# Optimization experiments

Hardware: AMD Instinct MI355X
Metric: run time of the kernel (lower is better)

## Reference

```python
import jax, jax.numpy as jnp
import numpy as np
from jax import lax

B, W, M = 4, 20, 512
RNN_HID = 64
N_HIDDEN = RNN_HID          # bi = False
HALF = N_HIDDEN // 2
K = 10
LONG_K = W // 2             # conv_long kernel
LONG_OUT = W - 2 * (LONG_K - 1)   # = 2
N_SPATIAL = 10


def setup_inputs() -> dict:
    key = jax.random.key(0)
    ks = jax.random.split(key, 24)
    g = lambda i, shape, s=0.05: jax.random.normal(ks[i], shape, jnp.float32) * s
    return {
        "x": jax.random.normal(ks[0], (B, W, M), jnp.float32),
        # vanilla RNN (tanh), 1 layer, input_size=1
        "W_ih": g(1, (RNN_HID, 1), 0.2), "W_hh": g(2, (RNN_HID, RNN_HID), 0.1),
        "b_ih": g(3, (RNN_HID,)), "b_hh": g(4, (RNN_HID,)),
        # attention adjacency params
        "W1": g(5, (HALF, N_HIDDEN), 0.1), "b1": g(6, (HALF,)),
        "W2": g(7, (HALF, N_HIDDEN), 0.1),
        "V": g(8, (HALF,), 0.1), "bv": g(9, (1,)),
        "Wb": g(10, (M, M), 0.05), "wb": g(11, (1,)),
        # conv / conv_long
        "conv_w": g(12, (K, 1, W), 0.1), "conv_b": g(13, (K,)),
        "convl_w": g(14, (K, 1, LONG_K), 0.1), "convl_b": g(15, (K,)),
        # graph conv layers: adj @ (x @ W) + b
        "gc1_w": g(16, ((1 + LONG_OUT) * K, N_HIDDEN), 0.1), "gc1_b": g(17, (N_HIDDEN,)),
        "gc2_w": g(18, (N_HIDDEN, N_SPATIAL), 0.1), "gc2_b": g(19, (N_SPATIAL,)),
        # output head
        "out_w": g(20, (1, N_HIDDEN + N_SPATIAL), 0.1), "out_b": g(21, (1,)),
        # fixed geographic adjacency (data.adj)
        "adj": jax.random.uniform(ks[22], (M, M), dtype=jnp.float32),
    }


def _conv1d(x, w, b, dilation=1):
    # x: (N, Cin, W), w: (Cout, Cin, K) -> (N, Cout, Wout), VALID padding
    y = lax.conv_general_dilated(x, w, (1,), 'VALID', rhs_dilation=(dilation,),
                                 dimension_numbers=('NCH', 'OIH', 'NCH'))
    return y + b[None, :, None]


def reference(x, W_ih, W_hh, b_ih, b_hh, W1, b1, W2, V, bv, Wb, wb,
              conv_w, conv_b, convl_w, convl_b, gc1_w, gc1_b, gc2_w, gc2_b,
              out_w, out_b, adj):
    b, w, m = x.shape
    # ---- RNN encode each node's scalar series: (b*m, w, 1) -> last hidden ----
    xr = jnp.transpose(x, (0, 2, 1)).reshape(b * m, w)          # (bm, w)
    inp = xr[..., None] @ W_ih.T + b_ih                         # (bm, w, H)

    def step(h, u):
        return jnp.tanh(u + h @ W_hh.T + b_hh), None

    h0 = jnp.zeros((b * m, RNN_HID), x.dtype)
    h_last, _ = lax.scan(step, h0, jnp.swapaxes(inp, 0, 1))     # (bm, H)
    last_hid = h_last.reshape(b, m, N_HIDDEN)
    out_temporal = last_hid

    # ---- pairwise bilinear attention adjacency (broadcast instead of repeat) ----
    p = last_hid @ W1.T                                         # (b, m, H/2)
    q = last_hid @ W2.T                                         # (b, m, H/2)
    e = jax.nn.elu(p[:, :, None, :] + q[:, None, :, :] + b1)    # (b, m, m, H/2)
    a_mx = e @ V + bv[0]                                        # (b, m, m)
    # F.normalize(p=2, dim=1)
    nrm = jnp.maximum(jnp.sqrt(jnp.sum(a_mx * a_mx, axis=1, keepdims=True)), 1e-12)
    a_mx = a_mx / nrm
    c = jax.nn.sigmoid(a_mx @ Wb + wb[0])                       # (b, m, m)
    A = adj[None] * c + a_mx * (1.0 - c)

    # ---- per-node convs, batched over all b*m series (no Python loop) ----
    h_tmp = xr[:, None, :]                                      # (bm, 1, w)
    r = _conv1d(h_tmp, conv_w, conv_b)                          # (bm, k, 1)
    r_long = _conv1d(h_tmp, convl_w, convl_b, dilation=2)       # (bm, k, long_out)
    r_l = jnp.concatenate([r, r_long], axis=-1).reshape(b, m, -1)  # (b, m, (1+lo)*k)
    r_l = jax.nn.relu(r_l)

    # ---- graph convolutions: adj @ (x @ W) + b ----
    xg = jax.nn.relu(A @ (r_l @ gc1_w) + gc1_b)                 # (b, m, H)
    out_spatial = jax.nn.relu(A @ (xg @ gc2_w) + gc2_b)         # (b, m, 10)

    out = jnp.concatenate([out_spatial, out_temporal], axis=-1)
    return (out @ out_w.T + out_b)[..., 0]                      # (b, m)
```

## Files before the change

kernel.cpp:

```cpp
#include <hip/hip_runtime.h>
#include <hip/hip_bf16.h>
#include <cstdint>
#include <cstddef>

#define OFF_P     0
#define OFF_QB    65536
#define OFF_TDOT  131072
#define OFF_COLSQ 133120
#define OFF_XGP   135168
#define OFF_AMXB  266240
#define OFF_ABF   790528
#define OFF_G1T   1314816
#define OFF_WBT   1380352

typedef __attribute__((ext_vector_type(8))) short short8;
typedef __attribute__((ext_vector_type(8))) unsigned short ushort8;
typedef __attribute__((ext_vector_type(4))) float f32x4;

__device__ inline unsigned short f2bf(float f) {
    unsigned u = __builtin_bit_cast(unsigned, f);
    unsigned r = u + 0x7FFFu + ((u >> 16) & 1u);
    return (unsigned short)(r >> 16);
}
__device__ inline unsigned short f2bf_fast(float f) {
    unsigned u = __builtin_bit_cast(unsigned, f);
    return (unsigned short)((u + 0x8000u) >> 16);
}
__device__ inline float bf2f(unsigned short s) {
    unsigned u = ((unsigned)s) << 16;
    return __builtin_bit_cast(float, u);
}
__device__ inline float tanh_fast(float x) {
    return 1.f - 2.f/(__expf(2.f*x) + 1.f);
}

__global__ __launch_bounds__(256) void k1_rnn(
    const float* __restrict__ x, const float* __restrict__ W_ih,
    const float* __restrict__ W_hh, const float* __restrict__ b_ih,
    const float* __restrict__ b_hh, const float* __restrict__ W1,
    const float* __restrict__ b1, const float* __restrict__ W2,
    const float* __restrict__ conv_w, const float* __restrict__ conv_b,
    const float* __restrict__ convl_w, const float* __restrict__ convl_b,
    const float* __restrict__ gc1_w, const float* __restrict__ out_w,
    const float* __restrict__ out_b, const float* __restrict__ Wb,
    float* __restrict__ p_out, float* __restrict__ qb_out,
    unsigned short* __restrict__ G1T, float* __restrict__ tdot,
    float* __restrict__ colsq, unsigned short* __restrict__ WbT)
{
    __shared__ float h_sh[4][64];
    __shared__ float xt_sh[4][20];
    __shared__ float rl_sh[4][30];
    __shared__ float tile[64][68];
    int tid = threadIdx.x;

    if (blockIdx.x >= 512) {
        int tt = blockIdx.x - 512;
        int k0 = (tt >> 3) * 64, j0 = (tt & 7) * 64;
        #pragma unroll
        for (int q = 0; q < 4; ++q) {
            int kr = (tid>>4) + 16*q;
            int jc = (tid&15)*4;
            *(float4*)&tile[kr][jc] = *(const float4*)(Wb + (size_t)(k0+kr)*512 + j0 + jc);
        }
        __syncthreads();
        int jl = tid>>2, kc = (tid&3)*16;
        int j = j0 + jl;
        ushort8 v0, v1;
        #pragma unroll
        for (int kk = 0; kk < 8; ++kk) v0[kk] = f2bf(tile[kc+kk][jl]);
        #pragma unroll
        for (int kk = 0; kk < 8; ++kk) v1[kk] = f2bf(tile[kc+8+kk][jl]);
        unsigned short* dst = WbT + (size_t)j*512 + k0 + kc;
        *(ushort8*)dst = v0;
        *(ushort8*)(dst+8) = v1;
        return;
    }

    int w = tid >> 6, lane = tid & 63;
    int s = blockIdx.x * 4 + w;
    int b = s >> 9, m = s & 511;

    if (blockIdx.x < 8) colsq[blockIdx.x * 256 + tid] = 0.f;

    if (lane < 20) xt_sh[w][lane] = x[(b*20 + lane)*512 + m];

    float wrow[64];
    const float* wr = W_hh + lane*64;
    #pragma unroll
    for (int k4 = 0; k4 < 16; ++k4) {
        float4 v = reinterpret_cast<const float4*>(wr)[k4];
        wrow[4*k4+0]=v.x; wrow[4*k4+1]=v.y; wrow[4*k4+2]=v.z; wrow[4*k4+3]=v.w;
    }
    float wih = W_ih[lane], bih = b_ih[lane], bhh = b_hh[lane];
    h_sh[w][lane] = 0.f;
    float h = 0.f;

    if (lane < 10) {
        float acc = conv_b[lane];
        #pragma unroll
        for (int t = 0; t < 20; ++t) acc += conv_w[lane*20+t]*xt_sh[w][t];
        rl_sh[w][3*lane] = fmaxf(acc, 0.f);
    } else if (lane < 30) {
        int idx = lane-10, j = idx>>1, oo = idx&1;
        float acc = convl_b[j];
        #pragma unroll
        for (int t = 0; t < 10; ++t) acc += convl_w[j*10+t]*xt_sh[w][oo+2*t];
        rl_sh[w][3*j+1+oo] = fmaxf(acc, 0.f);
    }

    for (int t = 0; t < 20; ++t) {
        float a0=0.f, a1=0.f, a2=0.f, a3=0.f;
        #pragma unroll
        for (int k = 0; k < 64; k += 4) {
            a0 += wrow[k+0]*h_sh[w][k+0];
            a1 += wrow[k+1]*h_sh[w][k+1];
            a2 += wrow[k+2]*h_sh[w][k+2];
            a3 += wrow[k+3]*h_sh[w][k+3];
        }
        float acc = xt_sh[w][t]*wih + bih + bhh + ((a0+a1)+(a2+a3));
        h = tanh_fast(acc);
        h_sh[w][lane] = h;
    }

    float td = h * out_w[10 + lane];
    #pragma unroll
    for (int off = 32; off; off >>= 1) td += __shfl_down(td, off);
    if (lane == 0) tdot[s] = td + out_b[0];

    if (lane < 32) {
        const float* w1r = W1 + lane*64;
        float acc = 0.f;
        #pragma unroll
        for (int k = 0; k < 64; ++k) acc += w1r[k]*h_sh[w][k];
        p_out[s*32 + lane] = acc;
    } else {
        int i = lane - 32;
        const float* w2r = W2 + i*64;
        float acc = 0.f;
        #pragma unroll
        for (int k = 0; k < 64; ++k) acc += w2r[k]*h_sh[w][k];
        qb_out[s*32 + i] = acc + b1[i];
    }

    float g = 0.f;
    #pragma unroll
    for (int t = 0; t < 30; ++t) g += rl_sh[w][t]*gc1_w[t*64 + lane];
    G1T[((size_t)(b*64 + lane))*512 + m] = f2bf(g);
}

__global__ __launch_bounds__(256) void k2_amx(
    const float* __restrict__ p, const float* __restrict__ qb,
    const float* __restrict__ V, const float* __restrict__ bv,
    unsigned short* __restrict__ amxB, float* __restrict__ colsq,
    float* __restrict__ xg_pre)
{
    __shared__ float p_sh[32*36], q_sh[32*36], v_sh[32], sq_sh[32*17];
    int t = threadIdx.x;
    int b = blockIdx.z, i0 = blockIdx.y*32, j0 = blockIdx.x*32;

    int fb = (blockIdx.z<<8) | (blockIdx.y<<4) | blockIdx.x;
    if (fb < 128) {
        float4 zz = {0.f,0.f,0.f,0.f};
        *(float4*)&xg_pre[(size_t)fb*1024 + t*4] = zz;
    }

    {
        int r = t >> 3, c4 = (t & 7)*4;
        *(float4*)&p_sh[r*36 + c4] = *(const float4*)(p  + (size_t)(b*512 + i0 + r)*32 + c4);
        *(float4*)&q_sh[r*36 + c4] = *(const float4*)(qb + (size_t)(b*512 + j0 + r)*32 + c4);
    }
    if (t < 32) v_sh[t] = V[t];
    __syncthreads();

    int ti = t >> 4, tj = t & 15;
    float bv0 = bv[0];
    float a00 = bv0, a01 = bv0, a10 = bv0, a11 = bv0;
    #pragma unroll
    for (int h = 0; h < 32; ++h) {
        float p0 = p_sh[ti*36 + h], p1 = p_sh[(ti+16)*36 + h];
        float q0 = q_sh[tj*36 + h], q1 = q_sh[(tj+16)*36 + h];
        float vh = v_sh[h];
        float x00 = p0+q0, x01 = p0+q1, x10 = p1+q0, x11 = p1+q1;
        float e00 = x00 > 0.f ? x00 : __expf(x00)-1.f;
        float e01 = x01 > 0.f ? x01 : __expf(x01)-1.f;
        float e10 = x10 > 0.f ? x10 : __expf(x10)-1.f;
        float e11 = x11 > 0.f ? x11 : __expf(x11)-1.f;
        a00 += vh*e00; a01 += vh*e01; a10 += vh*e10; a11 += vh*e11;
    }
    size_t base0 = ((size_t)(b*512 + i0 + ti))*512 + j0;
    size_t base1 = ((size_t)(b*512 + i0 + ti + 16))*512 + j0;
    amxB[base0 + tj]      = f2bf(a00);
    amxB[base0 + tj + 16] = f2bf(a01);
    amxB[base1 + tj]      = f2bf(a10);
    amxB[base1 + tj + 16] = f2bf(a11);

    sq_sh[tj*17 + ti]      = a00*a00 + a10*a10;
    sq_sh[(tj+16)*17 + ti] = a01*a01 + a11*a11;
    __syncthreads();
    if (t < 32) {
        float ssum = 0.f;
        #pragma unroll
        for (int r = 0; r < 16; ++r) ssum += sq_sh[t*17 + r];
        atomicAdd(&colsq[b*512 + j0 + t], ssum);
    }
}

__global__ __launch_bounds__(256) void k3_mfma(
    const unsigned short* __restrict__ amxB, const unsigned short* __restrict__ WbT,
    const unsigned short* __restrict__ G1T, const float* __restrict__ colsq,
    const float* __restrict__ wb, const float* __restrict__ adj,
    unsigned short* __restrict__ Abf, float* __restrict__ xg_pre)
{
    __shared__ unsigned short amx_save[4][32*40];
    __shared__ unsigned short Atr[4][32*40];
    int tid = threadIdx.x;
    int wv = tid >> 6, lane = tid & 63;
    int b = blockIdx.z;
    int i0 = blockIdx.y*32;
    int j0 = blockIdx.x*128 + wv*32;

    f32x4 acc[2][2] = {};

    int sl = (lane>>4)*8;
    int fr = lane & 15;
    const unsigned short* abase = amxB + ((size_t)(b*512 + i0 + fr))*512 + sl;
    const unsigned short* bbase = WbT  + ((size_t)(j0 + fr))*512 + sl;
    const float* csq = colsq + b*512 + sl;

    #pragma unroll 2
    for (int k0 = 0; k0 < 512; k0 += 32) {
        float4 c0 = *(const float4*)(csq + k0);
        float4 c1 = *(const float4*)(csq + k0 + 4);
        float iv[8] = {
            rsqrtf(fmaxf(c0.x,1e-24f)), rsqrtf(fmaxf(c0.y,1e-24f)),
            rsqrtf(fmaxf(c0.z,1e-24f)), rsqrtf(fmaxf(c0.w,1e-24f)),
            rsqrtf(fmaxf(c1.x,1e-24f)), rsqrtf(fmaxf(c1.y,1e-24f)),
            rsqrtf(fmaxf(c1.z,1e-24f)), rsqrtf(fmaxf(c1.w,1e-24f)) };

        short8 a0r = *(const short8*)(abase + k0);
        short8 a1r = *(const short8*)(abase + 16*512 + k0);
        short8 b0  = *(const short8*)(bbase + k0);
        short8 b1  = *(const short8*)(bbase + 16*512 + k0);

        if (k0 == j0) {
            *(short8*)&amx_save[wv][fr*40 + sl]      = a0r;
            *(short8*)&amx_save[wv][(fr+16)*40 + sl] = a1r;
        }

        short8 a0, a1;
        #pragma unroll
        for (int e = 0; e < 8; ++e) {
            a0[e] = (short)f2bf_fast(bf2f((unsigned short)a0r[e]) * iv[e]);
            a1[e] = (short)f2bf_fast(bf2f((unsigned short)a1r[e]) * iv[e]);
        }

        acc[0][0] = __builtin_amdgcn_mfma_f32_16x16x32_bf16(a0, b0, acc[0][0],0,0,0);
        acc[0][1] = __builtin_amdgcn_mfma_f32_16x16x32_bf16(a0, b1, acc[0][1],0,0,0);
        acc[1][0] = __builtin_amdgcn_mfma_f32_16x16x32_bf16(a1, b0, acc[1][0],0,0,0);
        acc[1][1] = __builtin_amdgcn_mfma_f32_16x16x32_bf16(a1, b1, acc[1][1],0,0,0);
    }

    float wbs = wb[0];
    #pragma unroll
    for (int fj = 0; fj < 2; ++fj) {
        int jl = fj*16 + fr;
        int j = j0 + jl;
        float inv = rsqrtf(fmaxf(colsq[b*512 + j], 1e-24f));
        #pragma unroll
        for (int fi = 0; fi < 2; ++fi)
        #pragma unroll
        for (int r = 0; r < 4; ++r) {
            int il = fi*16 + (lane>>4)*4 + r;
            float S = acc[fi][fj][r] + wbs;
            float c = 1.f/(1.f + __expf(-S));
            float aN = bf2f(amx_save[wv][il*40 + jl]) * inv;
            unsigned short u = f2bf(adj[(size_t)(i0+il)*512 + j]*c + aN*(1.f - c));
            Abf[((size_t)(b*512) + i0 + il)*512 + j] = u;
            Atr[wv][il*40 + jl] = u;
        }
    }

    short8 aT0 = *(const short8*)&Atr[wv][fr*40 + sl];
    short8 aT1 = *(const short8*)&Atr[wv][(fr+16)*40 + sl];
    f32x4 acc2[2][4] = {};
    #pragma unroll
    for (int cb = 0; cb < 4; ++cb) {
        short8 gfrag = *(const short8*)(G1T + ((size_t)(b*64 + cb*16 + fr))*512 + j0 + sl);
        acc2[0][cb] = __builtin_amdgcn_mfma_f32_16x16x32_bf16(aT0, gfrag, acc2[0][cb],0,0,0);
        acc2[1][cb] = __builtin_amdgcn_mfma_f32_16x16x32_bf16(aT1, gfrag, acc2[1][cb],0,0,0);
    }
    #pragma unroll
    for (int fi = 0; fi < 2; ++fi)
    #pragma unroll
    for (int cb = 0; cb < 4; ++cb)
    #pragma unroll
    for (int rr = 0; rr < 4; ++rr) {
        int i = i0 + fi*16 + (lane>>4)*4 + rr;
        int c = cb*16 + fr;
        atomicAdd(&xg_pre[((size_t)(b*512) + i)*64 + c], acc2[fi][cb][rr]);
    }
}

__global__ __launch_bounds__(256) void k4_out(
    const unsigned short* __restrict__ Abf, const float* __restrict__ xg_pre,
    const float* __restrict__ gc1_b, const float* __restrict__ gc2_w,
    const float* __restrict__ gc2_b, const float* __restrict__ out_w,
    const float* __restrict__ tdot, float* __restrict__ out)
{
    __shared__ float z_l[10*512];
    __shared__ float g2w[640];
    __shared__ float g1b[64];
    int t = threadIdx.x;
    int bid = blockIdx.x;
    int b = bid >> 6;
    int i0 = (bid & 63) * 8;

    for (int idx = t; idx < 640; idx += 256) g2w[idx] = gc2_w[idx];
    if (t < 64) g1b[t] = gc1_b[t];
    __syncthreads();

    {
        const float* xr0 = xg_pre + ((size_t)(b*512) + t)*64;
        const float* xr1 = xr0 + 256*64;
        float acc0[10] = {}, acc1[10] = {};
        #pragma unroll 4
        for (int c = 0; c < 64; c += 4) {
            float4 va = *(const float4*)(xr0 + c);
            float4 vb = *(const float4*)(xr1 + c);
            float aa[4] = {va.x,va.y,va.z,va.w};
            float bb[4] = {vb.x,vb.y,vb.z,vb.w};
            #pragma unroll
            for (int e = 0; e < 4; ++e) {
                float v0 = fmaxf(aa[e] + g1b[c+e], 0.f);
                float v1 = fmaxf(bb[e] + g1b[c+e], 0.f);
                #pragma unroll
                for (int sx = 0; sx < 10; ++sx) {
                    float wgt = g2w[(c+e)*10 + sx];
                    acc0[sx] += v0*wgt;
                    acc1[sx] += v1*wgt;
                }
            }
        }
        #pragma unroll
        for (int sx = 0; sx < 10; ++sx) {
            z_l[sx*512 + t]       = acc0[sx];
            z_l[sx*512 + t + 256] = acc1[sx];
        }
    }
    __syncthreads();

    int w = t >> 6, lane = t & 63;
    #pragma unroll
    for (int rep = 0; rep < 2; ++rep) {
        int s = b*512 + i0 + w*2 + rep;
        float a[8];
        #pragma unroll
        for (int q = 0; q < 8; ++q)
            a[q] = bf2f(Abf[(size_t)s*512 + q*64 + lane]);
        float acc[10];
        #pragma unroll
        for (int sx = 0; sx < 10; ++sx) {
            float ssum = 0.f;
            #pragma unroll
            for (int q = 0; q < 8; ++q) ssum += a[q]*z_l[sx*512 + q*64 + lane];
            acc[sx] = ssum;
        }
        #pragma unroll
        for (int sx = 0; sx < 10; ++sx)
            #pragma unroll
            for (int off = 32; off; off >>= 1) acc[sx] += __shfl_down(acc[sx], off);
        if (lane == 0) {
            float o = tdot[s];
            #pragma unroll
            for (int sx = 0; sx < 10; ++sx)
                o += fmaxf(acc[sx] + gc2_b[sx], 0.f) * out_w[sx];
            out[s] = o;
        }
    }
}

extern "C" void kernel_launch(void* const* d_in, const int* in_sizes, int n_in,
                              void* d_out, int out_size, void* d_ws, size_t ws_size,
                              hipStream_t stream) {
    const float* x       = (const float*)d_in[0];
    const float* W_ih    = (const float*)d_in[1];
    const float* W_hh    = (const float*)d_in[2];
    const float* b_ih    = (const float*)d_in[3];
    const float* b_hh    = (const float*)d_in[4];
    const float* W1      = (const float*)d_in[5];
    const float* b1      = (const float*)d_in[6];
    const float* W2      = (const float*)d_in[7];
    const float* V       = (const float*)d_in[8];
    const float* bv      = (const float*)d_in[9];
    const float* Wb      = (const float*)d_in[10];
    const float* wb      = (const float*)d_in[11];
    const float* conv_w  = (const float*)d_in[12];
    const float* conv_b  = (const float*)d_in[13];
    const float* convl_w = (const float*)d_in[14];
    const float* convl_b = (const float*)d_in[15];
    const float* gc1_w   = (const float*)d_in[16];
    const float* gc1_b   = (const float*)d_in[17];
    const float* gc2_w   = (const float*)d_in[18];
    const float* gc2_b   = (const float*)d_in[19];
    const float* out_w   = (const float*)d_in[20];
    const float* out_b   = (const float*)d_in[21];
    const float* adj     = (const float*)d_in[22];

    float* ws    = (float*)d_ws;
    float* p     = ws + OFF_P;
    float* qb    = ws + OFF_QB;
    float* tdot  = ws + OFF_TDOT;
    float* colsq = ws + OFF_COLSQ;
    float* xg_pre = ws + OFF_XGP;
    unsigned short* amxB = (unsigned short*)(ws + OFF_AMXB);
    unsigned short* Abf  = (unsigned short*)(ws + OFF_ABF);
    unsigned short* G1T  = (unsigned short*)(ws + OFF_G1T);
    unsigned short* WbT  = (unsigned short*)(ws + OFF_WBT);
    float* out   = (float*)d_out;

    k1_rnn<<<dim3(576), dim3(256), 0, stream>>>(
        x, W_ih, W_hh, b_ih, b_hh, W1, b1, W2,
        conv_w, conv_b, convl_w, convl_b, gc1_w, out_w, out_b, Wb,
        p, qb, G1T, tdot, colsq, WbT);

    k2_amx<<<dim3(16,16,4), dim3(256), 0, stream>>>(p, qb, V, bv, amxB, colsq, xg_pre);

    k3_mfma<<<dim3(4,16,4), dim3(256), 0, stream>>>(
        amxB, WbT, G1T, colsq, wb, adj, Abf, xg_pre);

    k4_out<<<dim3(256), dim3(256), 0, stream>>>(
        Abf, xg_pre, gc1_b, gc2_w, gc2_b, out_w, tdot, out);
}
```

Measured before the change: 68.90 us.

## Replace xg_pre atomics with per-column-block partial sums reduced in k4

k3 previously used global atomicAdd to accumulate A@G1 into xg_pre, which needed zeroing in k2. Now each block first reduces its four waves' results in shared memory, then writes a deterministic partial slab per column block. k4 sums the four partials when it loads them. k4's grid also shrinks from 256 to 64 blocks, each covering 32 rows, so the per-batch z computation is repeated fewer times. This adds partial-buffer traffic and an extra shared-memory reduction, and the smaller k4 grid lowers its parallelism.

```diff
diff --git a/kernel.cpp b/kernel.cpp
--- a/kernel.cpp
+++ b/kernel.cpp
@@ -8,10 +8,10 @@
 #define OFF_TDOT  131072
 #define OFF_COLSQ 133120
 #define OFF_XGP   135168
-#define OFF_AMXB  266240
-#define OFF_ABF   790528
-#define OFF_G1T   1314816
-#define OFF_WBT   1380352
+#define OFF_AMXB  659456
+#define OFF_ABF   1183744
+#define OFF_G1T   1708032
+#define OFF_WBT   1773568
 
 typedef __attribute__((ext_vector_type(8))) short short8;
 typedef __attribute__((ext_vector_type(8))) unsigned short ushort8;
@@ -151,19 +151,11 @@
 __global__ __launch_bounds__(256) void k2_amx(
     const float* __restrict__ p, const float* __restrict__ qb,
     const float* __restrict__ V, const float* __restrict__ bv,
-    unsigned short* __restrict__ amxB, float* __restrict__ colsq,
-    float* __restrict__ xg_pre)
+    unsigned short* __restrict__ amxB, float* __restrict__ colsq)
 {
     __shared__ float p_sh[32*36], q_sh[32*36], v_sh[32], sq_sh[32*17];
     int t = threadIdx.x;
     int b = blockIdx.z, i0 = blockIdx.y*32, j0 = blockIdx.x*32;
-
-    int fb = (blockIdx.z<<8) | (blockIdx.y<<4) | blockIdx.x;
-    if (fb < 128) {
-        float4 zz = {0.f,0.f,0.f,0.f};
-        *(float4*)&xg_pre[(size_t)fb*1024 + t*4] = zz;
-    }
-
     {
         int r = t >> 3, c4 = (t & 7)*4;
         *(float4*)&p_sh[r*36 + c4] = *(const float4*)(p  + (size_t)(b*512 + i0 + r)*32 + c4);
@@ -209,15 +201,17 @@
     const unsigned short* __restrict__ amxB, const unsigned short* __restrict__ WbT,
     const unsigned short* __restrict__ G1T, const float* __restrict__ colsq,
     const float* __restrict__ wb, const float* __restrict__ adj,
-    unsigned short* __restrict__ Abf, float* __restrict__ xg_pre)
+    unsigned short* __restrict__ Abf, float* __restrict__ xg_part)
 {
     __shared__ unsigned short amx_save[4][32*40];
     __shared__ unsigned short Atr[4][32*40];
+    __shared__ float xg_l[4][32*68];
     int tid = threadIdx.x;
     int wv = tid >> 6, lane = tid & 63;
     int b = blockIdx.z;
     int i0 = blockIdx.y*32;
-    int j0 = blockIdx.x*128 + wv*32;
+    int jb = blockIdx.x;
+    int j0 = jb*128 + wv*32;
 
     f32x4 acc[2][2] = {};
 
@@ -294,15 +288,29 @@
     #pragma unroll
     for (int cb = 0; cb < 4; ++cb)
     #pragma unroll
-    for (int rr = 0; rr < 4; ++rr) {
-        int i = i0 + fi*16 + (lane>>4)*4 + rr;
-        int c = cb*16 + fr;
-        atomicAdd(&xg_pre[((size_t)(b*512) + i)*64 + c], acc2[fi][cb][rr]);
+    for (int rr = 0; rr < 4; ++rr)
+        xg_l[wv][(fi*16 + (lane>>4)*4 + rr)*68 + cb*16 + fr] = acc2[fi][cb][rr];
+    __syncthreads();
+
+    {
+        int il = tid >> 3, c8 = (tid & 7)*8;
+        float4 s0 = *(const float4*)&xg_l[0][il*68 + c8];
+        float4 s1 = *(const float4*)&xg_l[0][il*68 + c8 + 4];
+        #pragma unroll
+        for (int v = 1; v < 4; ++v) {
+            float4 t0 = *(const float4*)&xg_l[v][il*68 + c8];
+            float4 t1 = *(const float4*)&xg_l[v][il*68 + c8 + 4];
+            s0.x += t0.x; s0.y += t0.y; s0.z += t0.z; s0.w += t0.w;
+            s1.x += t1.x; s1.y += t1.y; s1.z += t1.z; s1.w += t1.w;
+        }
+        float* dst = xg_part + ((size_t)(jb*4 + b)*512 + i0 + il)*64 + c8;
+        *(float4*)dst = s0;
+        *(float4*)(dst + 4) = s1;
     }
 }
 
 __global__ __launch_bounds__(256) void k4_out(
-    const unsigned short* __restrict__ Abf, const float* __restrict__ xg_pre,
+    const unsigned short* __restrict__ Abf, const float* __restrict__ xg_part,
     const float* __restrict__ gc1_b, const float* __restrict__ gc2_w,
     const float* __restrict__ gc2_b, const float* __restrict__ out_w,
     const float* __restrict__ tdot, float* __restrict__ out)
@@ -312,47 +320,49 @@
     __shared__ float g1b[64];
     int t = threadIdx.x;
     int bid = blockIdx.x;
-    int b = bid >> 6;
-    int i0 = (bid & 63) * 8;
+    int b = bid >> 4;
+    int i0 = (bid & 15) * 32;
 
     for (int idx = t; idx < 640; idx += 256) g2w[idx] = gc2_w[idx];
     if (t < 64) g1b[t] = gc1_b[t];
     __syncthreads();
 
-    {
-        const float* xr0 = xg_pre + ((size_t)(b*512) + t)*64;
-        const float* xr1 = xr0 + 256*64;
-        float acc0[10] = {}, acc1[10] = {};
-        #pragma unroll 4
-        for (int c = 0; c < 64; c += 4) {
-            float4 va = *(const float4*)(xr0 + c);
-            float4 vb = *(const float4*)(xr1 + c);
-            float aa[4] = {va.x,va.y,va.z,va.w};
-            float bb[4] = {vb.x,vb.y,vb.z,vb.w};
+    #pragma unroll
+    for (int rep = 0; rep < 2; ++rep) {
+        int jj = t + rep*256;
+        const float* base = xg_part + ((size_t)(b*512) + jj)*64;
+        float4 sum[16];
+        #pragma unroll
+        for (int c4 = 0; c4 < 16; ++c4) sum[c4] = *(const float4*)(base + c4*4);
+        #pragma unroll
+        for (int v = 1; v < 4; ++v) {
+            const float* bv_ = base + (size_t)v*131072;
+            #pragma unroll
+            for (int c4 = 0; c4 < 16; ++c4) {
+                float4 q = *(const float4*)(bv_ + c4*4);
+                sum[c4].x += q.x; sum[c4].y += q.y; sum[c4].z += q.z; sum[c4].w += q.w;
+            }
+        }
+        float acc[10] = {};
+        #pragma unroll
+        for (int c4 = 0; c4 < 16; ++c4) {
+            float vv[4] = {sum[c4].x, sum[c4].y, sum[c4].z, sum[c4].w};
             #pragma unroll
             for (int e = 0; e < 4; ++e) {
-                float v0 = fmaxf(aa[e] + g1b[c+e], 0.f);
-                float v1 = fmaxf(bb[e] + g1b[c+e], 0.f);
+                float v = fmaxf(vv[e] + g1b[c4*4 + e], 0.f);
                 #pragma unroll
-                for (int sx = 0; sx < 10; ++sx) {
-                    float wgt = g2w[(c+e)*10 + sx];
-                    acc0[sx] += v0*wgt;
-                    acc1[sx] += v1*wgt;
-                }
+                for (int sx = 0; sx < 10; ++sx)
+                    acc[sx] += v * g2w[(c4*4 + e)*10 + sx];
             }
         }
         #pragma unroll
-        for (int sx = 0; sx < 10; ++sx) {
-            z_l[sx*512 + t]       = acc0[sx];
-            z_l[sx*512 + t + 256] = acc1[sx];
-        }
+        for (int sx = 0; sx < 10; ++sx) z_l[sx*512 + jj] = acc[sx];
     }
     __syncthreads();
 
     int w = t >> 6, lane = t & 63;
-    #pragma unroll
-    for (int rep = 0; rep < 2; ++rep) {
-        int s = b*512 + i0 + w*2 + rep;
+    for (int rr = 0; rr < 8; ++rr) {
+        int s = b*512 + i0 + w*8 + rr;
         float a[8];
         #pragma unroll
         for (int q = 0; q < 8; ++q)
@@ -411,7 +421,7 @@
     float* qb    = ws + OFF_QB;
     float* tdot  = ws + OFF_TDOT;
     float* colsq = ws + OFF_COLSQ;
-    float* xg_pre = ws + OFF_XGP;
+    float* xg_part = ws + OFF_XGP;
     unsigned short* amxB = (unsigned short*)(ws + OFF_AMXB);
     unsigned short* Abf  = (unsigned short*)(ws + OFF_ABF);
     unsigned short* G1T  = (unsigned short*)(ws + OFF_G1T);
@@ -423,11 +433,11 @@
         conv_w, conv_b, convl_w, convl_b, gc1_w, out_w, out_b, Wb,
         p, qb, G1T, tdot, colsq, WbT);
 
-    k2_amx<<<dim3(16,16,4), dim3(256), 0, stream>>>(p, qb, V, bv, amxB, colsq, xg_pre);
+    k2_amx<<<dim3(16,16,4), dim3(256), 0, stream>>>(p, qb, V, bv, amxB, colsq);
 
     k3_mfma<<<dim3(4,16,4), dim3(256), 0, stream>>>(
-        amxB, WbT, G1T, colsq, wb, adj, Abf, xg_pre);
-
-    k4_out<<<dim3(256), dim3(256), 0, stream>>>(
-        Abf, xg_pre, gc1_b, gc2_w, gc2_b, out_w, tdot, out);
-}
+        amxB, WbT, G1T, colsq, wb, adj, Abf, xg_part);
+
+    k4_out<<<dim3(64), dim3(256), 0, stream>>>(
+        Abf, xg_part, gc1_b, gc2_w, gc2_b, out_w, tdot, out);
+}
```

After: 91.83 us. 1.33x slower.
